# Optimization experiments

Measured on AMD Instinct MI355X. Metric: run time of the kernel, lower is better.

## Reference

```python
import jax, jax.numpy as jnp
import numpy as np

BATCH, SEQ, D_IN, D_HID, N_CLS = 256, 128, 1024, 2048, 1024


def setup_inputs() -> dict:
    key = jax.random.key(0)
    ks = jax.random.split(key, 6)
    s_in = 1.0 / np.sqrt(D_IN)
    s_hid = 1.0 / np.sqrt(D_HID)
    return {
        "x": jax.random.normal(ks[0], (BATCH, SEQ, D_IN), dtype=jnp.float32),
        "W_hx": jax.random.normal(ks[1], (D_HID, D_IN), dtype=jnp.float32) * s_in,
        "W_hh": jax.random.normal(ks[2], (D_HID, D_HID), dtype=jnp.float32) * s_hid,
        "W_ph": jax.random.normal(ks[3], (N_CLS, D_HID), dtype=jnp.float32) * s_hid,
        "b_h": jax.random.normal(ks[4], (D_HID,), dtype=jnp.float32) * 0.01,
        "b_p": jax.random.normal(ks[5], (N_CLS,), dtype=jnp.float32) * 0.01,
    }


def reference(x, W_hx, W_hh, W_ph, b_h, b_p):
    # Input projection for all timesteps in one large GEMM: [B,S,Din] @ [Din,H] -> [B,S,H]
    xproj = jnp.einsum("bsd,hd->bsh", x, W_hx) + b_h  # bias folded in once per step
    h0 = jnp.zeros((x.shape[0], W_hh.shape[0]), dtype=x.dtype)

    def step(h_prev, xp_t):
        # h_t = W_hx x_t + W_hh h_prev + b_h (linear recurrence, as in source)
        h_t = xp_t + h_prev @ W_hh.T
        return h_t, None

    # scan over time axis: xproj transposed to [S,B,H]
    h_T, _ = jax.lax.scan(step, h0, jnp.swapaxes(xproj, 0, 1))
    # readout from final hidden state: p = W_ph h_T + b_p -> [B, C]
    p = h_T @ W_ph.T + b_p
    return p
```

## Files before the change

kernel.cpp:

```cpp
#include <hip/hip_runtime.h>
#include <stdint.h>

#define B_SZ   256
#define SEQ_LEN 128
#define DIN    1024
#define DHID   2048
#define NCLS   1024
#define NBLK   256
#define NROUND 8

typedef unsigned short ushort_t;
typedef short bf16x8 __attribute__((ext_vector_type(8)));
typedef float f32x16 __attribute__((ext_vector_type(16)));
typedef ushort_t u16x8 __attribute__((ext_vector_type(8)));

__device__ __forceinline__ ushort_t f32_to_bf16(float f) {
  uint32_t u = __builtin_bit_cast(uint32_t, f);
  u = (u + 0x7FFFu + ((u >> 16) & 1u)) >> 16;
  return (ushort_t)u;
}
__device__ __forceinline__ float bf16_to_f32(ushort_t h) {
  uint32_t u = ((uint32_t)h) << 16;
  return __builtin_bit_cast(float, u);
}

__device__ __forceinline__ void llds16(const ushort_t* g, ushort_t* l) {
  __builtin_amdgcn_global_load_lds(
      (const __attribute__((address_space(1))) void*)g,
      (__attribute__((address_space(3))) void*)l, 16, 0, 0);
}

__device__ __forceinline__ void cstore_f32(float* p, float v) {
  __hip_atomic_store(p, v, __ATOMIC_RELAXED, __HIP_MEMORY_SCOPE_AGENT);
}
__device__ __forceinline__ void cstore_u64(void* p, uint64_t v) {
  __hip_atomic_store((uint64_t*)p, v, __ATOMIC_RELAXED, __HIP_MEMORY_SCOPE_AGENT);
}
__device__ __forceinline__ uint64_t cload_u64(const void* p) {
  return __hip_atomic_load((const uint64_t*)p, __ATOMIC_RELAXED, __HIP_MEMORY_SCOPE_AGENT);
}
__device__ __forceinline__ void cstore_u32(unsigned* p, unsigned v) {
  __hip_atomic_store(p, v, __ATOMIC_RELAXED, __HIP_MEMORY_SCOPE_AGENT);
}
__device__ __forceinline__ unsigned cload_u32(const unsigned* p) {
  return __hip_atomic_load(p, __ATOMIC_RELAXED, __HIP_MEMORY_SCOPE_AGENT);
}

__device__ __forceinline__ void gsync(unsigned* flags, unsigned ep) {
  __syncthreads();
  if (threadIdx.x == 0) cstore_u32(&flags[blockIdx.x], ep);
  if (threadIdx.x < 64) {
    const unsigned* f = flags + threadIdx.x * 4;
    for (;;) {
      unsigned a = cload_u32(f + 0), b = cload_u32(f + 1);
      unsigned c = cload_u32(f + 2), d = cload_u32(f + 3);
      bool ok = (a >= ep) & (b >= ep) & (c >= ep) & (d >= ep);
      if (__ballot(ok) == ~0ull) break;
      __builtin_amdgcn_s_sleep(1);
    }
  }
  __syncthreads();
}

__global__ void k_splitT(const float* __restrict__ src, ushort_t* __restrict__ hi,
                         ushort_t* __restrict__ lo, ushort_t* __restrict__ hiT,
                         ushort_t* __restrict__ loT) {
  __shared__ ushort_t th[64][65];
  __shared__ ushort_t tl[64][65];
  const int bx = blockIdx.x * 64, by = blockIdx.y * 64;
  const int c = threadIdx.x & 63, r0 = (threadIdx.x >> 6) * 16;
#pragma unroll
  for (int i = 0; i < 16; ++i) {
    size_t o = (size_t)(by + r0 + i) * DHID + bx + c;
    float v = src[o];
    ushort_t hh = f32_to_bf16(v);
    ushort_t ll = f32_to_bf16(v - bf16_to_f32(hh));
    hi[o] = hh;
    lo[o] = ll;
    th[r0 + i][c] = hh;
    tl[r0 + i][c] = ll;
  }
  __syncthreads();
#pragma unroll
  for (int i = 0; i < 16; ++i) {
    size_t o = (size_t)(bx + r0 + i) * DHID + by + c;
    hiT[o] = th[c][r0 + i];
    loT[o] = tl[c][r0 + i];
  }
}

__global__ void k_trb2(const ushort_t* __restrict__ sA, ushort_t* __restrict__ dA,
                       const ushort_t* __restrict__ sB, ushort_t* __restrict__ dB) {
  __shared__ ushort_t ta[64][65];
  __shared__ ushort_t tb[64][65];
  const int bx = blockIdx.x * 64, by = blockIdx.y * 64;
  const int c = threadIdx.x & 63, r0 = (threadIdx.x >> 6) * 16;
#pragma unroll
  for (int i = 0; i < 16; ++i) {
    size_t o = (size_t)(by + r0 + i) * DHID + bx + c;
    ta[r0 + i][c] = sA[o];
    tb[r0 + i][c] = sB[o];
  }
  __syncthreads();
#pragma unroll
  for (int i = 0; i < 16; ++i) {
    size_t o = (size_t)(bx + r0 + i) * DHID + by + c;
    dA[o] = ta[c][r0 + i];
    dB[o] = tb[c][r0 + i];
  }
}

__global__ void k_cvtW(const float* __restrict__ src, ushort_t* __restrict__ d,
                       ushort_t* __restrict__ dT) {
  __shared__ ushort_t t[64][65];
  const int bx = blockIdx.x * 64, by = blockIdx.y * 64;
  const int c = threadIdx.x & 63, r0 = (threadIdx.x >> 6) * 16;
#pragma unroll
  for (int i = 0; i < 16; ++i) {
    size_t o = (size_t)(by + r0 + i) * DIN + bx + c;
    ushort_t hh = f32_to_bf16(src[o]);
    d[o] = hh;
    t[r0 + i][c] = hh;
  }
  __syncthreads();
#pragma unroll
  for (int i = 0; i < 16; ++i)
    dT[(size_t)(bx + r0 + i) * DHID + by + c] = t[c][r0 + i];
}

__global__ void k_cvt(const float* __restrict__ s, ushort_t* __restrict__ d, int n4) {
  int i = blockIdx.x * 256 + threadIdx.x;
  if (i >= n4) return;
  float4 v = ((const float4*)s)[i];
  ushort4 hv;
  hv.x = f32_to_bf16(v.x); hv.y = f32_to_bf16(v.y);
  hv.z = f32_to_bf16(v.z); hv.w = f32_to_bf16(v.w);
  ((ushort4*)d)[i] = hv;
}

__global__ void k_cvtT(const float* __restrict__ s, ushort_t* __restrict__ d) {
  int i = blockIdx.x * 256 + threadIdx.x;
  int dd = (i & (DIN / 8 - 1)) * 8;
  int bs = i >> 7;
  int b = bs >> 7;
  int t = bs & (SEQ_LEN - 1);
  const float* src = s + (size_t)bs * DIN + dd;
  float4 v0 = *(const float4*)src;
  float4 v1 = *(const float4*)(src + 4);
  u16x8 hv;
  hv[0] = f32_to_bf16(v0.x); hv[1] = f32_to_bf16(v0.y);
  hv[2] = f32_to_bf16(v0.z); hv[3] = f32_to_bf16(v0.w);
  hv[4] = f32_to_bf16(v1.x); hv[5] = f32_to_bf16(v1.y);
  hv[6] = f32_to_bf16(v1.z); hv[7] = f32_to_bf16(v1.w);
  *(u16x8*)(d + ((size_t)t * B_SZ + b) * DIN + dd) = hv;
}

__global__ void k_bvec(const float* __restrict__ W, const float* __restrict__ b,
                       float* __restrict__ out) {
  int row = (blockIdx.x * blockDim.x + threadIdx.x) >> 6;
  int lane = threadIdx.x & 63;
  if (row >= DHID) return;
  float s = 0.0f;
  for (int j = lane; j < DHID; j += 64) s += W[(size_t)row * DHID + j] * b[j];
#pragma unroll
  for (int off = 32; off; off >>= 1) s += __shfl_down(s, off);
  if (lane == 0) out[row] = b[row] + s;
}

struct BigArgs {
  const ushort_t* A[3];
  const ushort_t* B[3];
  int nseg;
  int klen;
  size_t tA, sA;
  size_t ldo;
  const ushort_t* D;
  size_t tD;
  const float* bias;
  ushort_t* out_hi;
  ushort_t* out_lo;
  int lognx;
};

__device__ __forceinline__ void big_epi(const BigArgs& a, f32x16 (&acc)[2][2],
                                        int bm0, int bn0) {
  const int tid = threadIdx.x, lane = tid & 63, wv = tid >> 6;
  const int l31 = lane & 31, half = lane >> 5;
  int gm0 = bm0 + (wv & 1) * 64, gn0 = bn0 + (wv >> 1) * 64;
#pragma unroll
  for (int mi = 0; mi < 2; ++mi)
#pragma unroll
    for (int ni = 0; ni < 2; ++ni)
#pragma unroll
      for (int r = 0; r < 16; ++r) {
        int row = gm0 + mi * 32 + (r & 3) + 8 * (r >> 2) + 4 * half;
        int col = gn0 + ni * 32 + l31;
        float v = acc[mi][ni][r];
        if (a.bias) v += a.bias[col];
        if (a.D)
          v += bf16_to_f32(a.D[(size_t)(row >> 8) * a.tD +
                               (size_t)(row & 255) * 2048 + col]);
        ushort_t hh = f32_to_bf16(v);
        a.out_hi[(size_t)row * a.ldo + col] = hh;
        if (a.out_lo)
          a.out_lo[(size_t)row * a.ldo + col] = f32_to_bf16(v - bf16_to_f32(hh));
      }
}

__device__ __forceinline__ void big_body_db(const BigArgs& a, int wg) {
  __shared__ __align__(16) ushort_t lds[32768];
  const int tid = threadIdx.x, lane = tid & 63, wv = tid >> 6;
  const int l31 = lane & 31, half = lane >> 5;

  const int bn0 = (wg & ((1 << a.lognx) - 1)) * 128;
  const int bm0 = (wg >> a.lognx) * 128;
  const int t_ = bm0 >> 8, mrem = bm0 & 255;
  const int kit = a.klen >> 6;

  f32x16 acc[2][2];
#pragma unroll
  for (int p = 0; p < 2; ++p)
#pragma unroll
    for (int q = 0; q < 2; ++q)
#pragma unroll
      for (int r = 0; r < 16; ++r) acc[p][q][r] = 0.0f;

  auto stage = [&](int buf, int i) {
    int seg = 0, ii = i;
    while (ii >= kit) { ii -= kit; ++seg; }
    const int kc = ii * 64;
    const ushort_t* Ab = a.A[seg];
    const ushort_t* Bb = a.B[seg];
#pragma unroll
    for (int j = 0; j < 4; ++j) {
      int s = tid + 256 * j;
      int prow = s >> 3, glc = (s & 7) ^ (prow & 7);
      llds16(Ab + (size_t)t_ * a.tA + (size_t)(mrem + prow) * a.sA + (kc + glc * 8),
             &lds[(size_t)(buf * 16384 + (wv * 64 + 256 * j) * 16) / 2]);
      llds16(Bb + (size_t)(bn0 + prow) * a.klen + (kc + glc * 8),
             &lds[(size_t)(32768 + buf * 16384 + (wv * 64 + 256 * j) * 16) / 2]);
    }
  };

  const int nit = a.nseg * kit;
  stage(0, 0);
  for (int i = 0; i < nit; ++i) {
    int buf = i & 1;
    if (i + 1 < nit) {
      stage(buf ^ 1, i + 1);
      __builtin_amdgcn_s_waitcnt(0x3FF0 | 8);
    } else {
      __builtin_amdgcn_s_waitcnt(0x3FF0);
    }
    __builtin_amdgcn_s_barrier();
    const ushort_t* At = &lds[buf * 8192];
    const ushort_t* Bt = &lds[16384 + buf * 8192];
#pragma unroll
    for (int ks = 0; ks < 4; ++ks) {
      int ch = ks * 2 + half;
      bf16x8 af[2], bf_[2];
#pragma unroll
      for (int mi = 0; mi < 2; ++mi) {
        int row = (wv & 1) * 64 + mi * 32 + l31;
        int pch = ch ^ (row & 7);
        af[mi] = *(const bf16x8*)&At[row * 64 + pch * 8];
      }
#pragma unroll
      for (int ni = 0; ni < 2; ++ni) {
        int row = (wv >> 1) * 64 + ni * 32 + l31;
        int pch = ch ^ (row & 7);
        bf_[ni] = *(const bf16x8*)&Bt[row * 64 + pch * 8];
      }
#pragma unroll
      for (int mi = 0; mi < 2; ++mi)
#pragma unroll
        for (int ni = 0; ni < 2; ++ni)
          acc[mi][ni] = __builtin_amdgcn_mfma_f32_32x32x16_bf16(
              af[mi], bf_[ni], acc[mi][ni], 0, 0, 0);
    }
    __builtin_amdgcn_s_barrier();
  }
  big_epi(a, acc, bm0, bn0);
}

__device__ __forceinline__ void big_body_sb(const BigArgs& a, int wg) {
  __shared__ __align__(16) ushort_t lds[16384];
  const int tid = threadIdx.x, lane = tid & 63, wv = tid >> 6;
  const int l31 = lane & 31, half = lane >> 5;

  const int bn0 = (wg & ((1 << a.lognx) - 1)) * 128;
  const int bm0 = (wg >> a.lognx) * 128;
  const int t_ = bm0 >> 8, mrem = bm0 & 255;
  const int kit = a.klen >> 6;

  f32x16 acc[2][2];
#pragma unroll
  for (int p = 0; p < 2; ++p)
#pragma unroll
    for (int q = 0; q < 2; ++q)
#pragma unroll
      for (int r = 0; r < 16; ++r) acc[p][q][r] = 0.0f;

  auto stage = [&](int i) {
    int seg = 0, ii = i;
    while (ii >= kit) { ii -= kit; ++seg; }
    const int kc = ii * 64;
    const ushort_t* Ab = a.A[seg];
    const ushort_t* Bb = a.B[seg];
#pragma unroll
    for (int j = 0; j < 4; ++j) {
      int s = tid + 256 * j;
      int prow = s >> 3, glc = (s & 7) ^ (prow & 7);
      llds16(Ab + (size_t)t_ * a.tA + (size_t)(mrem + prow) * a.sA + (kc + glc * 8),
             &lds[(size_t)((wv * 64 + 256 * j) * 16) / 2]);
      llds16(Bb + (size_t)(bn0 + prow) * a.klen + (kc + glc * 8),
             &lds[(size_t)(16384 + (wv * 64 + 256 * j) * 16) / 2]);
    }
  };

  const int nit = a.nseg * kit;
  for (int i = 0; i < nit; ++i) {
    stage(i);
    __builtin_amdgcn_s_waitcnt(0x3FF0);
    __builtin_amdgcn_s_barrier();
    const ushort_t* At = &lds[0];
    const ushort_t* Bt = &lds[8192];
#pragma unroll
    for (int ks = 0; ks < 4; ++ks) {
      int ch = ks * 2 + half;
      bf16x8 af[2], bf_[2];
#pragma unroll
      for (int mi = 0; mi < 2; ++mi) {
        int row = (wv & 1) * 64 + mi * 32 + l31;
        int pch = ch ^ (row & 7);
        af[mi] = *(const bf16x8*)&At[row * 64 + pch * 8];
      }
#pragma unroll
      for (int ni = 0; ni < 2; ++ni) {
        int row = (wv >> 1) * 64 + ni * 32 + l31;
        int pch = ch ^ (row & 7);
        bf_[ni] = *(const bf16x8*)&Bt[row * 64 + pch * 8];
      }
#pragma unroll
      for (int mi = 0; mi < 2; ++mi)
#pragma unroll
        for (int ni = 0; ni < 2; ++ni)
          acc[mi][ni] = __builtin_amdgcn_mfma_f32_32x32x16_bf16(
              af[mi], bf_[ni], acc[mi][ni], 0, 0, 0);
    }
    __builtin_amdgcn_s_barrier();
  }
  big_epi(a, acc, bm0, bn0);
}

__global__ __launch_bounds__(256, 1) void k_big2(BigArgs a0, BigArgs a1, int nblk0) {
  int wg = blockIdx.x;
  if (wg < nblk0) {
    big_body_db(a0, wg);
  } else {
    big_body_db(a1, wg - nblk0);
  }
}

__global__ __launch_bounds__(256, 4) void k_big1s(BigArgs a) {
  big_body_sb(a, blockIdx.x);
}
__global__ __launch_bounds__(256, 4) void k_big2s(BigArgs a0, BigArgs a1, int nblk0) {
  int wg = blockIdx.x;
  if (wg < nblk0) {
    big_body_sb(a0, wg);
  } else {
    big_body_sb(a1, wg - nblk0);
  }
}

__global__ __launch_bounds__(512, 2) void k_rnn(
    const ushort_t* __restrict__ w_hi, const ushort_t* __restrict__ w_lo,
    ushort_t* __restrict__ h_hi, ushort_t* __restrict__ h_lo,
    const ushort_t* __restrict__ z_hi, const ushort_t* __restrict__ z_lo,
    float* __restrict__ P, unsigned* __restrict__ flags) {
  __shared__ __align__(16) ushort_t lds[81920];
  char* ldsb = (char*)&lds[0];

  const int tid = threadIdx.x, lane = tid & 63, wv = tid >> 6;
  const int l31 = lane & 31, half = lane >> 5;
  const int kslice = wv & 1, mq = (wv >> 1) & 1, nq = wv >> 2;
  const int b = blockIdx.x;
  const int kb = b & 7, nb = (b >> 3) & 15, mb = b >> 7;
  const int n0 = nb * 128, k0 = kb * 256, m0 = mb * 128;

#pragma unroll
  for (int hl = 0; hl < 2; ++hl) {
    const ushort_t* W = hl ? w_lo : w_hi;
    for (int p = 0; p < 4; ++p)
#pragma unroll
      for (int j = 0; j < 2; ++j) {
        int s = tid + 512 * j;
        int prow = s >> 3, glc = (s & 7) ^ (prow & 7);
        const ushort_t* g = W + (size_t)(n0 + prow) * DHID + (k0 + p * 64 + glc * 8);
        ushort_t* d = (ushort_t*)(ldsb + hl * 65536 + p * 16384 + (wv * 64 + 512 * j) * 16);
        llds16(g, d);
      }
  }
  __builtin_amdgcn_s_waitcnt(0x3FF0);
  __syncthreads();

  const int srow0 = wv * 16 + (lane >> 4);
  const int skk   = 4 * (lane & 15);
  const int sg    = (lane & 15) >> 1;
  const int ssub  = lane & 1;

  uint64_t R[4][4];

  auto regload = [&](int slot, int c) {
    const ushort_t* src = (c < 4) ? h_hi : h_lo;
    const int p = c & 3;
#pragma unroll
    for (int i = 0; i < 4; ++i)
      R[slot][i] = cload_u64(src + (size_t)(m0 + srow0 + 4 * i) * DHID +
                             (k0 + p * 64 + skk));
  };
  auto dswrite = [&](int buf, int slot) {
#pragma unroll
    for (int i = 0; i < 4; ++i) {
      int lr = srow0 + 4 * i;
      *(uint64_t*)(ldsb + 131072 + buf * 16384 + lr * 128 +
                   ((sg ^ (lr & 7)) * 16) + ssub * 8) = R[slot][i];
    }
  };

  auto phaseB = [&](ushort4 zq, ushort4 zl, bool withP) {
    const int r = b;
    const int c0 = tid * 4;
    float v[4] = {bf16_to_f32(zq.x) + bf16_to_f32(zl.x),
                  bf16_to_f32(zq.y) + bf16_to_f32(zl.y),
                  bf16_to_f32(zq.z) + bf16_to_f32(zl.z),
                  bf16_to_f32(zq.w) + bf16_to_f32(zl.w)};
    if (withP) {
#pragma unroll
      for (int k = 0; k < 8; ++k) {
        const float* pp = P + ((size_t)k * B_SZ + r) * DHID + c0;
#pragma unroll
        for (int j = 0; j < 2; ++j) {
          uint64_t q = cload_u64((const uint64_t*)pp + j);
          float2 f = __builtin_bit_cast(float2, q);
          v[2 * j]     += f.x;
          v[2 * j + 1] += f.y;
        }
      }
    }
    ushort_t hh[4], ll[4];
#pragma unroll
    for (int e = 0; e < 4; ++e) {
      hh[e] = f32_to_bf16(v[e]);
      ll[e] = f32_to_bf16(v[e] - bf16_to_f32(hh[e]));
    }
    uint64_t q0, q1;
    __builtin_memcpy(&q0, &hh[0], 8);
    __builtin_memcpy(&q1, &ll[0], 8);
    cstore_u64(h_hi + (size_t)r * DHID + c0, q0);
    cstore_u64(h_lo + (size_t)r * DHID + c0, q1);
  };

  unsigned ep = 1;
  {
    ushort4 zq = *(const ushort4*)(z_hi + (size_t)b * DHID + tid * 4);
    ushort4 zl = *(const ushort4*)(z_lo + (size_t)b * DHID + tid * 4);
    phaseB(zq, zl, false);
  }
  gsync(flags, ep); ++ep;

  for (int j = 1; j < NROUND; ++j) {
    f32x16 acc[2][2];
#pragma unroll
    for (int p = 0; p < 2; ++p)
#pragma unroll
      for (int q = 0; q < 2; ++q)
#pragma unroll
        for (int r = 0; r < 16; ++r) acc[p][q][r] = 0.0f;

    regload(0, 0); regload(1, 1); regload(2, 2); regload(3, 3);
    dswrite(0, 0);
    __syncthreads();

    for (int c = 0; c < 8; ++c) {
      if (c + 4 <= 7) regload(c & 3, c + 4);
      if (c + 1 <= 7) dswrite((c + 1) & 1, (c + 1) & 3);

      const char* At = ldsb + 131072 + (c & 1) * 16384;
      const char* Bh = ldsb + (size_t)(c & 3) * 16384;
      const char* Bl = ldsb + 65536 + (size_t)(c & 3) * 16384;
      const bool isHi = c < 4;
#pragma unroll
      for (int ks = 0; ks < 2; ++ks) {
        const int g = (kslice * 2 + ks) * 2 + half;
        bf16x8 af[2], bh_[2], bl_[2];
#pragma unroll
        for (int mi = 0; mi < 2; ++mi) {
          int row = mq * 64 + mi * 32 + l31;
          af[mi] = *(const bf16x8*)(At + row * 128 + (g ^ (row & 7)) * 16);
        }
#pragma unroll
        for (int ni = 0; ni < 2; ++ni) {
          int row = nq * 64 + ni * 32 + l31;
          int off = row * 128 + (g ^ (row & 7)) * 16;
          bh_[ni] = *(const bf16x8*)(Bh + off);
          if (isHi) bl_[ni] = *(const bf16x8*)(Bl + off);
        }
#pragma unroll
        for (int mi = 0; mi < 2; ++mi)
#pragma unroll
          for (int ni = 0; ni < 2; ++ni) {
            acc[mi][ni] = __builtin_amdgcn_mfma_f32_32x32x16_bf16(
                af[mi], bh_[ni], acc[mi][ni], 0, 0, 0);
            if (isHi)
              acc[mi][ni] = __builtin_amdgcn_mfma_f32_32x32x16_bf16(
                  af[mi], bl_[ni], acc[mi][ni], 0, 0, 0);
          }
      }
      __syncthreads();
    }

    {
      float* scr = (float*)(ldsb + 131072);
      const int pr = mq * 2 + nq;
#pragma unroll
      for (int r = 0; r < 2; ++r) {
        if (kslice == 1) {
#pragma unroll
          for (int ni = 0; ni < 2; ++ni)
#pragma unroll
            for (int reg = 0; reg < 16; ++reg) {
              int row32 = (reg & 3) + 8 * (reg >> 2) + 4 * half;
              scr[pr * 2048 + row32 * 64 + ni * 32 + l31] = acc[r][ni][reg];
            }
        }
        __syncthreads();
        if (kslice == 0) {
#pragma unroll
          for (int ni = 0; ni < 2; ++ni)
#pragma unroll
            for (int reg = 0; reg < 16; ++reg) {
              int row32 = (reg & 3) + 8 * (reg >> 2) + 4 * half;
              acc[r][ni][reg] += scr[pr * 2048 + row32 * 64 + ni * 32 + l31];
            }
        }
        __syncthreads();
      }
    }

    if (kslice == 0) {
      float* Pt = P + (size_t)kb * (B_SZ * DHID);
#pragma unroll
      for (int mi = 0; mi < 2; ++mi)
#pragma unroll
        for (int ni = 0; ni < 2; ++ni)
#pragma unroll
          for (int reg = 0; reg < 16; ++reg) {
            int row = m0 + mq * 64 + mi * 32 + (reg & 3) + 8 * (reg >> 2) + 4 * half;
            int col = n0 + nq * 64 + ni * 32 + l31;
            cstore_f32(&Pt[(size_t)row * DHID + col], acc[mi][ni][reg]);
          }
    }
    ushort4 zq = *(const ushort4*)(z_hi + ((size_t)j * 256 + b) * DHID + tid * 4);
    ushort4 zl = *(const ushort4*)(z_lo + ((size_t)j * 256 + b) * DHID + tid * 4);
    gsync(flags, ep); ++ep;

    phaseB(zq, zl, true);
    gsync(flags, ep); ++ep;
  }
}

struct Seg {
  const ushort_t* A;
  const ushort_t* B;
  int a_stride;
  int b_stride;
  int k_len;
};
struct Args {
  Seg seg[4];
  int n_seg;
  int n_iters;
  const float* bias;
  ushort_t* out_hi;
  ushort_t* out_lo;
  float* out_f32;
  int ldo;
};

#define DEPTH 6
__global__ __launch_bounds__(256, 1) void k_gemm(Args args) {
  __shared__ __align__(16) char pool[DEPTH * 12288];
  const int tid = threadIdx.x, lane = tid & 63, wv = tid >> 6;
  const int bm0 = blockIdx.y * 32, bn0 = blockIdx.x * 64;

  f32x16 acc[2];
#pragma unroll
  for (int c = 0; c < 2; ++c)
#pragma unroll
    for (int r = 0; r < 16; ++r) acc[c][r] = 0.0f;

  const int prow0 = tid >> 3;
  const int glc0 = (tid & 7) ^ (prow0 & 7);
  const int prow1 = (tid + 256) >> 3;
  const int glc1 = (tid & 7) ^ (prow1 & 7);

  auto stage = [&](int buf, const Seg& sg, int k0) {
    const ushort_t* ga = sg.A + (size_t)(bm0 + prow0) * sg.a_stride + (k0 + glc0 * 8);
    const ushort_t* gb0 = sg.B + (size_t)(bn0 + prow0) * sg.b_stride + (k0 + glc0 * 8);
    const ushort_t* gb1 = sg.B + (size_t)(bn0 + prow1) * sg.b_stride + (k0 + glc1 * 8);
    ushort_t* la = (ushort_t*)(pool + buf * 12288) + wv * 512;
    ushort_t* lb = (ushort_t*)(pool + buf * 12288 + 4096) + wv * 512;
    llds16(ga, la);
    llds16(gb0, lb);
    llds16(gb1, lb + 2048);
  };

  const int nit = args.n_iters;
  int sc = 0, kc = 0;
  int nst = nit < (DEPTH - 1) ? nit : (DEPTH - 1);
  for (int s = 0; s < nst; ++s) {
    stage(s, args.seg[sc], kc);
    kc += 64;
    if (kc >= args.seg[sc].k_len) { kc = 0; ++sc; }
  }

  const int half = lane >> 5, l31 = lane & 31;
  const int lch = wv * 2 + half;
  int sb = DEPTH - 1, cb = 0;

  for (int i = 0; i < nit; ++i) {
    int ahead = nit - 1 - i;
    if (ahead > DEPTH - 1) ahead = DEPTH - 1;
    if (i + DEPTH - 1 < nit) {
      stage(sb, args.seg[sc], kc);
      if (++sb == DEPTH) sb = 0;
      kc += 64;
      if (kc >= args.seg[sc].k_len) { kc = 0; ++sc; }
    }
    switch (ahead) {
      case 5: __builtin_amdgcn_s_waitcnt(0x3FF0 | 15); break;
      case 4: __builtin_amdgcn_s_waitcnt(0x3FF0 | 12); break;
      case 3: __builtin_amdgcn_s_waitcnt(0x3FF0 | 9); break;
      case 2: __builtin_amdgcn_s_waitcnt(0x3FF0 | 6); break;
      case 1: __builtin_amdgcn_s_waitcnt(0x3FF0 | 3); break;
      default: __builtin_amdgcn_s_waitcnt(0x3FF0 | 0); break;
    }
    __builtin_amdgcn_s_barrier();

    const ushort_t* tA = (const ushort_t*)(pool + cb * 12288);
    const ushort_t* tB = tA + 2048;
    bf16x8 af, bfm[2];
    {
      int row = l31;
      int pch = lch ^ (row & 7);
      af = *(const bf16x8*)&tA[row * 64 + pch * 8];
    }
#pragma unroll
    for (int ni = 0; ni < 2; ++ni) {
      int row = ni * 32 + l31;
      int pch = lch ^ (row & 7);
      bfm[ni] = *(const bf16x8*)&tB[row * 64 + pch * 8];
    }
#pragma unroll
    for (int ni = 0; ni < 2; ++ni)
      acc[ni] = __builtin_amdgcn_mfma_f32_32x32x16_bf16(af, bfm[ni], acc[ni], 0, 0, 0);

    if (++cb == DEPTH) cb = 0;
    __builtin_amdgcn_s_barrier();
  }

  __syncthreads();
  float* red = (float*)pool + wv * 2048;
#pragma unroll
  for (int ni = 0; ni < 2; ++ni)
#pragma unroll
    for (int r = 0; r < 16; ++r) {
      int row = (r & 3) + 8 * (r >> 2) + 4 * half;
      int col = ni * 32 + l31;
      red[row * 64 + col] = acc[ni][r];
    }
  __syncthreads();

  const float* r0 = (const float*)pool;
  const float* r1 = r0 + 2048;
  const float* r2 = r0 + 4096;
  const float* r3 = r0 + 6144;
#pragma unroll
  for (int j = 0; j < 8; ++j) {
    int e = j * 256 + tid;
    int row = e >> 6, col = e & 63;
    float v = r0[e] + r1[e] + r2[e] + r3[e] + args.bias[bn0 + col];
    size_t o = (size_t)(bm0 + row) * args.ldo + (bn0 + col);
    if (args.out_f32) {
      args.out_f32[o] = v;
    } else {
      ushort_t h = f32_to_bf16(v);
      args.out_hi[o] = h;
      args.out_lo[o] = f32_to_bf16(v - bf16_to_f32(h));
    }
  }
}

extern "C" void kernel_launch(void* const* d_in, const int* in_sizes, int n_in,
                              void* d_out, int out_size, void* d_ws, size_t ws_size,
                              hipStream_t stream) {
  const float* x   = (const float*)d_in[0];
  const float* Whx = (const float*)d_in[1];
  const float* Whh = (const float*)d_in[2];
  const float* Wph = (const float*)d_in[3];
  const float* bh  = (const float*)d_in[4];
  const float* bp  = (const float*)d_in[5];

  const size_t WSZ = (size_t)DHID * DHID * 2;
  char* p = (char*)d_ws;
  ushort_t* whh_hi = (ushort_t*)p; p += WSZ;
  ushort_t* whh_lo = (ushort_t*)p; p += WSZ;
  ushort_t* whhT_hi= (ushort_t*)p; p += WSZ;
  ushort_t* whhT_lo= (ushort_t*)p; p += WSZ;
  ushort_t* w2_hi  = (ushort_t*)p; p += WSZ;
  ushort_t* w2_lo  = (ushort_t*)p; p += WSZ;
  ushort_t* w2T_hi = (ushort_t*)p; p += WSZ;
  ushort_t* w2T_lo = (ushort_t*)p; p += WSZ;
  ushort_t* w4_hi  = (ushort_t*)p; p += WSZ;
  ushort_t* w4_lo  = (ushort_t*)p; p += WSZ;
  ushort_t* w4T_hi = (ushort_t*)p; p += WSZ;
  ushort_t* w4T_lo = (ushort_t*)p; p += WSZ;
  ushort_t* w8_hi  = (ushort_t*)p; p += WSZ;
  ushort_t* w8_lo  = (ushort_t*)p; p += WSZ;
  ushort_t* w8T_hi = (ushort_t*)p; p += WSZ;
  ushort_t* w8T_lo = (ushort_t*)p; p += WSZ;
  ushort_t* w16_hi = (ushort_t*)p; p += WSZ;
  ushort_t* w16_lo = (ushort_t*)p; p += WSZ;
  ushort_t* whx_b  = (ushort_t*)p; p += (size_t)DHID * DIN * 2;
  ushort_t* whxT   = (ushort_t*)p; p += (size_t)DIN * DHID * 2;
  ushort_t* wa_b   = (ushort_t*)p; p += (size_t)DHID * DIN * 2;
  ushort_t* wph_b  = (ushort_t*)p; p += (size_t)NCLS * DHID * 2;
  ushort_t* xT     = (ushort_t*)p; p += (size_t)B_SZ * SEQ_LEN * DIN * 2;
  ushort_t* z2_b   = (ushort_t*)p; p += (size_t)64 * B_SZ * DHID * 2;
  ushort_t* z4_b   = (ushort_t*)p; p += (size_t)32 * B_SZ * DHID * 2;
  ushort_t* z8_b   = (ushort_t*)p; p += (size_t)16 * B_SZ * DHID * 2;
  ushort_t* z8_lo  = (ushort_t*)p; p += (size_t)16 * B_SZ * DHID * 2;
  ushort_t* z16_b  = (ushort_t*)p; p += (size_t)8 * B_SZ * DHID * 2;
  ushort_t* z16_lo = (ushort_t*)p; p += (size_t)8 * B_SZ * DHID * 2;
  float*    Part   = (float*)p;    p += (size_t)8 * B_SZ * DHID * 4;
  ushort_t* h_hi   = (ushort_t*)p; p += (size_t)B_SZ * DHID * 2;
  ushort_t* h_lo   = (ushort_t*)p; p += (size_t)B_SZ * DHID * 2;
  float*    b2_ws  = (float*)p;    p += (size_t)DHID * 4;
  unsigned* flags  = (unsigned*)p; p += NBLK * 4;

  hipMemsetAsync(flags, 0, NBLK * 4, stream);

  k_splitT<<<dim3(32, 32), 256, 0, stream>>>(Whh, whh_hi, whh_lo, whhT_hi, whhT_lo);
  {
    int n4 = NCLS * DHID / 4;
    k_cvt<<<(n4 + 255) / 256, 256, 0, stream>>>(Wph, wph_b, n4);
  }
  k_cvtT<<<(B_SZ * SEQ_LEN * DIN / 8) / 256, 256, 0, stream>>>(x, xT);
  k_cvtW<<<dim3(DIN / 64, DHID / 64), 256, 0, stream>>>(Whx, whx_b, whxT);
  k_bvec<<<512, 256, 0, stream>>>(Whh, bh, b2_ws);

  const size_t TBLK = (size_t)512 * DHID;

  BigArgs aWa = {};
  aWa.A[0] = whh_hi; aWa.B[0] = whxT;
  aWa.A[1] = whh_lo; aWa.B[1] = whxT;
  aWa.nseg = 2; aWa.klen = DHID; aWa.tA = (size_t)256 * DHID; aWa.sA = DHID;
  aWa.ldo = DIN; aWa.out_hi = wa_b; aWa.lognx = 3;

  BigArgs aW2 = {};
  aW2.A[0] = whh_hi; aW2.B[0] = whhT_hi;
  aW2.A[1] = whh_hi; aW2.B[1] = whhT_lo;
  aW2.A[2] = whh_lo; aW2.B[2] = whhT_hi;
  aW2.nseg = 3; aW2.klen = DHID; aW2.tA = (size_t)256 * DHID; aW2.sA = DHID;
  aW2.ldo = 2048; aW2.out_hi = w2_hi; aW2.out_lo = w2_lo; aW2.lognx = 4;

  BigArgs az2 = {};
  az2.A[0] = xT;              az2.B[0] = wa_b;
  az2.A[1] = xT + (size_t)B_SZ * DIN; az2.B[1] = whx_b;
  az2.nseg = 2; az2.klen = DIN;
  az2.tA = (size_t)2 * B_SZ * DIN; az2.sA = DIN;
  az2.ldo = 2048; az2.bias = b2_ws; az2.out_hi = z2_b; az2.lognx = 4;

  BigArgs aW4 = {};
  aW4.A[0] = w2_hi; aW4.B[0] = w2T_hi;
  aW4.A[1] = w2_hi; aW4.B[1] = w2T_lo;
  aW4.A[2] = w2_lo; aW4.B[2] = w2T_hi;
  aW4.nseg = 3; aW4.klen = DHID; aW4.tA = (size_t)256 * DHID; aW4.sA = DHID;
  aW4.ldo = 2048; aW4.out_hi = w4_hi; aW4.out_lo = w4_lo; aW4.lognx = 4;

  BigArgs az4 = {};
  az4.A[0] = z2_b; az4.B[0] = w2_hi; az4.nseg = 1; az4.klen = DHID;
  az4.tA = TBLK; az4.sA = DHID;
  az4.D = z2_b + (size_t)256 * DHID; az4.tD = TBLK;
  az4.ldo = 2048; az4.out_hi = z4_b; az4.lognx = 4;

  BigArgs aW8 = {};
  aW8.A[0] = w4_hi; aW8.B[0] = w4T_hi;
  aW8.A[1] = w4_hi; aW8.B[1] = w4T_lo;
  aW8.A[2] = w4_lo; aW8.B[2] = w4T_hi;
  aW8.nseg = 3; aW8.klen = DHID; aW8.tA = (size_t)256 * DHID; aW8.sA = DHID;
  aW8.ldo = 2048; aW8.out_hi = w8_hi; aW8.out_lo = w8_lo; aW8.lognx = 4;

  BigArgs az8 = {};
  az8.A[0] = z4_b; az8.B[0] = w4_hi; az8.nseg = 1; az8.klen = DHID;
  az8.tA = TBLK; az8.sA = DHID;
  az8.D = z4_b + (size_t)256 * DHID; az8.tD = TBLK;
  az8.ldo = 2048; az8.out_hi = z8_b; az8.out_lo = z8_lo; az8.lognx = 4;

  BigArgs aW16 = {};
  aW16.A[0] = w8_hi; aW16.B[0] = w8T_hi;
  aW16.A[1] = w8_hi; aW16.B[1] = w8T_lo;
  aW16.A[2] = w8_lo; aW16.B[2] = w8T_hi;
  aW16.nseg = 3; aW16.klen = DHID; aW16.tA = (size_t)256 * DHID; aW16.sA = DHID;
  aW16.ldo = 2048; aW16.out_hi = w16_hi; aW16.out_lo = w16_lo; aW16.lognx = 4;

  BigArgs az16 = {};
  az16.A[0] = z8_b;  az16.B[0] = w8_hi;
  az16.A[1] = z8_b;  az16.B[1] = w8_lo;
  az16.A[2] = z8_lo; az16.B[2] = w8_hi;
  az16.nseg = 3; az16.klen = DHID; az16.tA = TBLK; az16.sA = DHID;
  az16.D = z8_b + (size_t)256 * DHID; az16.tD = TBLK;
  az16.ldo = 2048; az16.out_hi = z16_b; az16.out_lo = z16_lo; az16.lognx = 4;

  k_big2<<<dim3(384), 256, 0, stream>>>(aW2, aWa, 256);
  k_big1s<<<dim3(2048), 256, 0, stream>>>(az2);
  k_trb2<<<dim3(32, 32), 256, 0, stream>>>(w2_hi, w2T_hi, w2_lo, w2T_lo);
  k_big2s<<<dim3(1280), 256, 0, stream>>>(aW4, az4, 256);
  k_trb2<<<dim3(32, 32), 256, 0, stream>>>(w4_hi, w4T_hi, w4_lo, w4T_lo);
  k_big2s<<<dim3(768), 256, 0, stream>>>(aW8, az8, 256);
  k_trb2<<<dim3(32, 32), 256, 0, stream>>>(w8_hi, w8T_hi, w8_lo, w8T_lo);
  k_big2<<<dim3(512), 256, 0, stream>>>(aW16, az16, 256);

  k_rnn<<<dim3(NBLK), 512, 0, stream>>>(w16_hi, w16_lo, h_hi, h_lo,
                                        z16_b, z16_lo, Part, flags);

  {
    Args a = {};
    a.seg[0] = { h_hi, wph_b, DHID, DHID, DHID };
    a.seg[1] = { h_lo, wph_b, DHID, DHID, DHID };
    a.n_seg = 2; a.n_iters = 2 * DHID / 64;
    a.bias = bp; a.out_hi = nullptr; a.out_lo = nullptr;
    a.out_f32 = (float*)d_out; a.ldo = NCLS;
    k_gemm<<<dim3(NCLS / 64, B_SZ / 32), 256, 0, stream>>>(a);
  }
}
```

Baseline: 994.7 us.

## Add 256x256-tile GEMM kernel for the z2 input projection

Introduces a new 512-thread GEMM kernel that computes 256x256 output tiles with 8 waves, each doing 4x2 32x32 MFMA blocks. It uses a double-buffered LDS layout split into four 16-wide K quarters, with a swizzle. The z2 projection launch moves from the 128-tile single-buffer kernel (2048 blocks) to this kernel (512 blocks). The aim is more operand reuse per global load and less global traffic. The trade-off is fewer blocks, heavier register use, and an epilogue that does scattered scalar stores.

```diff
diff --git a/kernel.cpp b/kernel.cpp
--- a/kernel.cpp
+++ b/kernel.cpp
@@ -372,6 +372,111 @@
   } else {
     big_body_sb(a1, wg - nblk0);
   }
+}
+
+__global__ __launch_bounds__(512, 2) void k_big256(BigArgs a) {
+  __shared__ __align__(16) ushort_t lds[65536];
+  char* ldsb = (char*)&lds[0];
+  const int tid = threadIdx.x, lane = tid & 63, w = tid >> 6;
+  const int l31 = lane & 31, half = lane >> 5;
+  const int wr = w >> 2, wc = w & 3;
+
+  const int bn0 = (blockIdx.x & ((1 << a.lognx) - 1)) * 256;
+  const int bm0 = (blockIdx.x >> a.lognx) * 256;
+  const int t_ = bm0 >> 8;
+  const int kit = a.klen >> 6;
+  const int nit = a.nseg * kit;
+
+  f32x16 acc[4][2];
+#pragma unroll
+  for (int mi = 0; mi < 4; ++mi)
+#pragma unroll
+    for (int ni = 0; ni < 2; ++ni)
+#pragma unroll
+      for (int r = 0; r < 16; ++r) acc[mi][ni][r] = 0.0f;
+
+  const int srow = tid >> 1;
+  const int sgc = (tid & 1) ^ ((srow >> 1) & 1);
+
+  auto stageg = [&](int b, int i, int q) {
+    int seg = 0, ii = i;
+    while (ii >= kit) { ii -= kit; ++seg; }
+    const int kc = ii * 64 + q * 16 + sgc * 8;
+    llds16(a.A[seg] + (size_t)t_ * a.tA + (size_t)srow * a.sA + kc,
+           (ushort_t*)(ldsb + (b << 16) + (q << 14) + (w << 10)));
+    llds16(a.B[seg] + (size_t)(bn0 + srow) * a.klen + kc,
+           (ushort_t*)(ldsb + (b << 16) + (q << 14) + 8192 + (w << 10)));
+  };
+
+  auto compute = [&](int b, int q) {
+    const char* Aq = ldsb + (b << 16) + (q << 14);
+    const char* Bq = Aq + 8192;
+    bf16x8 af[4], bf_[2];
+#pragma unroll
+    for (int mi = 0; mi < 4; ++mi) {
+      int row = wr * 128 + mi * 32 + l31;
+      af[mi] = *(const bf16x8*)(Aq + row * 32 + ((half ^ ((row >> 1) & 1)) << 4));
+    }
+#pragma unroll
+    for (int ni = 0; ni < 2; ++ni) {
+      int row = wc * 64 + ni * 32 + l31;
+      bf_[ni] = *(const bf16x8*)(Bq + row * 32 + ((half ^ ((row >> 1) & 1)) << 4));
+    }
+#pragma unroll
+    for (int mi = 0; mi < 4; ++mi)
+#pragma unroll
+      for (int ni = 0; ni < 2; ++ni)
+        acc[mi][ni] = __builtin_amdgcn_mfma_f32_32x32x16_bf16(
+            af[mi], bf_[ni], acc[mi][ni], 0, 0, 0);
+  };
+
+  stageg(0, 0, 0); stageg(0, 0, 1); stageg(0, 0, 2); stageg(0, 0, 3);
+  __builtin_amdgcn_s_waitcnt(0x3FF0 | 6);
+  __builtin_amdgcn_s_barrier();
+
+  for (int t = 0; t < nit - 1; ++t) {
+    int b = t & 1;
+#pragma unroll
+    for (int q = 0; q < 4; ++q) {
+      stageg(b ^ 1, t + 1, q);
+      compute(b, q);
+      __builtin_amdgcn_s_waitcnt(0x3FF0 | 6);
+      __builtin_amdgcn_s_barrier();
+    }
+  }
+  {
+    int b = (nit - 1) & 1;
+    compute(b, 0);
+    __builtin_amdgcn_s_waitcnt(0x3FF0 | 4);
+    __builtin_amdgcn_s_barrier();
+    compute(b, 1);
+    __builtin_amdgcn_s_waitcnt(0x3FF0 | 2);
+    __builtin_amdgcn_s_barrier();
+    compute(b, 2);
+    __builtin_amdgcn_s_waitcnt(0x3FF0);
+    __builtin_amdgcn_s_barrier();
+    compute(b, 3);
+  }
+
+  int gm0 = bm0 + wr * 128, gn0 = bn0 + wc * 64;
+#pragma unroll
+  for (int mi = 0; mi < 4; ++mi)
+#pragma unroll
+    for (int ni = 0; ni < 2; ++ni)
+#pragma unroll
+      for (int r = 0; r < 16; ++r) {
+        int row = gm0 + mi * 32 + (r & 3) + 8 * (r >> 2) + 4 * half;
+        int col = gn0 + ni * 32 + l31;
+        float v = acc[mi][ni][r];
+        if (a.bias) v += a.bias[col];
+        if (a.D)
+          v += bf16_to_f32(a.D[(size_t)(row >> 8) * a.tD +
+                               (size_t)(row & 255) * 2048 + col]);
+        ushort_t hh = f32_to_bf16(v);
+        a.out_hi[(size_t)row * a.ldo + col] = hh;
+        if (a.out_lo)
+          a.out_lo[(size_t)row * a.ldo + col] = f32_to_bf16(v - bf16_to_f32(hh));
+      }
 }
 
 __global__ __launch_bounds__(512, 2) void k_rnn(
@@ -781,7 +886,8 @@
   az2.A[1] = xT + (size_t)B_SZ * DIN; az2.B[1] = whx_b;
   az2.nseg = 2; az2.klen = DIN;
   az2.tA = (size_t)2 * B_SZ * DIN; az2.sA = DIN;
-  az2.ldo = 2048; az2.bias = b2_ws; az2.out_hi = z2_b; az2.lognx = 4;
+  az2.ldo = 2048; az2.bias = b2_ws; az2.out_hi = z2_b;
+  az2.lognx = 3;
 
   BigArgs aW4 = {};
   aW4.A[0] = w2_hi; aW4.B[0] = w2T_hi;
@@ -825,7 +931,7 @@
   az16.ldo = 2048; az16.out_hi = z16_b; az16.out_lo = z16_lo; az16.lognx = 4;
 
   k_big2<<<dim3(384), 256, 0, stream>>>(aW2, aWa, 256);
-  k_big1s<<<dim3(2048), 256, 0, stream>>>(az2);
+  k_big256<<<dim3(512), 512, 0, stream>>>(az2);
   k_trb2<<<dim3(32, 32), 256, 0, stream>>>(w2_hi, w2T_hi, w2_lo, w2T_lo);
   k_big2s<<<dim3(1280), 256, 0, stream>>>(aW4, az4, 256);
   k_trb2<<<dim3(32, 32), 256, 0, stream>>>(w4_hi, w4T_hi, w4_lo, w4T_lo);
```

After: 1.010 ms. No clear change (+1.6%).
